# Kernel tuning notes

Measured on AMD Instinct MI355X. Metric: run time of the kernel, lower is better.

Reference implementation:

```python
import jax, jax.numpy as jnp
import numpy as np

B, N, M12, H, O, I, DIFF = 8192, 100, 12, 64, 128, 12, 1.0
TWO_PI = 2.0 * np.pi


def _moments_single(xi, K):
    # xi: [N, 2] single sample; K: [12, 2] exponent pairs -> [12]
    xc = xi - xi.mean(axis=0)                 # center per-sample (mean over points)
    p = xc[:, None, :] ** K[None, :, :]       # [N, 12, 2]
    return jnp.sum(p[..., 0] * p[..., 1], axis=0)  # [12]


def setup_inputs() -> dict:
    key = jax.random.key(0)
    ks = jax.random.split(key, 8)
    # 12 integer central-moment exponent pairs (p, q)
    P = jnp.array([1, 2, 0, 2, 1, 3, 0, 2, 3, 1, 4, 0], jnp.float32)
    Q = jnp.array([1, 0, 2, 1, 2, 0, 3, 2, 1, 3, 0, 4], jnp.float32)
    K = jnp.stack([P, Q], axis=-1)            # [12, 2]

    x = jax.random.normal(ks[0], (B, N, 2), jnp.float32)
    t = jax.random.uniform(ks[1], (1,), jnp.float32, 0.1, 1.0)  # positive time
    W_fourier = jax.random.normal(ks[2], (H // 2,), jnp.float32) * 30.0

    def lin(k, fin, fout):
        bound = 1.0 / np.sqrt(fin)
        kw, kb = jax.random.split(k)
        W = jax.random.uniform(kw, (fin, fout), jnp.float32, -bound, bound)
        b = jax.random.uniform(kb, (fout,), jnp.float32, -bound, bound)
        return W, b

    embed_W, embed_b = lin(ks[3], H, H)
    lin1_W, lin1_b = lin(ks[4], I, H)
    lin2a_W, lin2a_b = lin(ks[5], H, O)
    lin2b_W, lin2b_b = lin(ks[6], O, I)
    lin2c_W, lin2c_b = lin(ks[7], I, I)
    return {
        'x': x, 't': t, 'K': K, 'W_fourier': W_fourier,
        'embed_W': embed_W, 'embed_b': embed_b,
        'lin1_W': lin1_W, 'lin1_b': lin1_b,
        'lin2a_W': lin2a_W, 'lin2a_b': lin2a_b,
        'lin2b_W': lin2b_W, 'lin2b_b': lin2b_b,
        'lin2c_W': lin2c_W, 'lin2c_b': lin2c_b,
    }


def reference(x, t, K, W_fourier, embed_W, embed_b, lin1_W, lin1_b,
              lin2a_W, lin2a_b, lin2b_W, lin2b_b, lin2c_W, lin2c_b):
    # Invariance encoding ('Moment' mode): [B, 12]
    m = jax.vmap(_moments_single, in_axes=(0, None))(x, K)
    h = jax.nn.gelu(m @ lin1_W + lin1_b, approximate=False)   # [B, H] (dropout = eval identity)
    # Gaussian Fourier time embedding: [1, H]
    xp = t[:, None] * W_fourier[None, :] * TWO_PI
    emb = jnp.concatenate([jnp.sin(xp), jnp.cos(xp)], axis=-1) @ embed_W + embed_b
    h = jax.nn.gelu((h + emb) @ lin2a_W + lin2a_b, approximate=False)
    h = jax.nn.gelu(h @ lin2b_W + lin2b_b, approximate=False)
    h = (h @ lin2c_W + lin2c_b) / jnp.sqrt(DIFF * t)          # [B, 12]
    # Per-sample jacobian of the moment map: [B, 12, N, 2]
    # (equals the block diagonal of torch.autograd.functional.jacobian over the batch)
    jac = jax.vmap(jax.jacrev(_moments_single), in_axes=(0, None))(x, K)
    # Replaces the (i, j) double loop of tiny matmuls with one batched contraction
    return jnp.einsum('bk,bknj->bnj', h, jac)                 # [B, N, 2]
```

## Files before the change

kernel.cpp:

```cpp
#include <hip/hip_runtime.h>
#include <hip/hip_bf16.h>


static __device__ __forceinline__ float gelu_f(float x) {
    float y = 0.7071067811865475f * x;
    float s = fabsf(y);
    float t = __builtin_amdgcn_rcpf(fmaf(0.3275911f, s, 1.0f));
    float p = t * fmaf(t, fmaf(t, fmaf(t, fmaf(t, 1.061405429f,
                    -1.453152027f), 1.421413741f), -0.284496736f), 0.254829592f);
    float e = __expf(-y * y);
    float ea = fmaf(-p, e, 1.0f);
    float erfv = copysignf(ea, y);
    return 0.5f * x * (1.0f + erfv);
}

#define DPP_ADD(v, ctrl) \
    v += __int_as_float(__builtin_amdgcn_update_dpp(0, __float_as_int(v), ctrl, 0xf, 0xf, true))

static __device__ __forceinline__ float wave_sum(float v) {
    DPP_ADD(v, 0x111);
    DPP_ADD(v, 0x112);
    DPP_ADD(v, 0x114);
    DPP_ADD(v, 0x118);
    DPP_ADD(v, 0x142);
    DPP_ADD(v, 0x143);
    return __int_as_float(__builtin_amdgcn_readlane(__float_as_int(v), 63));
}

#define TWO_PI_F 6.283185307179586f

__global__ __launch_bounds__(256) void scorenet_fused(
    const float* __restrict__ x,
    const float* __restrict__ t_in,
    const float* __restrict__ Wf,
    const float* __restrict__ embW,
    const float* __restrict__ embB,
    const float* __restrict__ W1,
    const float* __restrict__ b1,
    const float* __restrict__ W2a,
    const float* __restrict__ b2a,
    const float* __restrict__ W2b,
    const float* __restrict__ b2b,
    const float* __restrict__ W2c,
    const float* __restrict__ b2c,
    float* __restrict__ out,
    int B)
{
    __shared__ float s_f[64];
    __shared__ float s_emb[64];

    const int tid = threadIdx.x;
    const float tval = t_in[0];

    if (tid < 32) {
        float xp = tval * Wf[tid] * TWO_PI_F;
        s_f[tid]      = sinf(xp);
        s_f[tid + 32] = cosf(xp);
    }
    __syncthreads();
    if (tid < 64) {
        float acc = embB[tid];
        const float4* f4 = reinterpret_cast<const float4*>(s_f);
        #pragma unroll
        for (int c = 0; c < 16; ++c) {
            float4 a4 = f4[c];
            int j = 4 * c;
            acc = fmaf(a4.x, embW[(j+0)*64 + tid],
                  fmaf(a4.y, embW[(j+1)*64 + tid],
                  fmaf(a4.z, embW[(j+2)*64 + tid],
                  fmaf(a4.w, embW[(j+3)*64 + tid], acc))));
        }
        s_emb[tid] = acc;
    }
    __syncthreads();

    const int lane = tid & 63;
    const int b = blockIdx.x * 4 + (tid >> 6);
    if (b >= B) return;

    const float2* px = reinterpret_cast<const float2*>(x) + (size_t)b * 100;
    const bool has2 = lane < 36;

    float2 p0 = px[lane];
    float2 p1 = px[has2 ? lane + 64 : lane];
    float xa = p0.x, ya = p0.y;
    float xb = has2 ? p1.x : 0.0f;
    float yb = has2 ? p1.y : 0.0f;

    const float mux = wave_sum(xa + xb) * 0.01f;
    const float muy = wave_sum(ya + yb) * 0.01f;

    float ua = xa - mux, va = ya - muy;
    float ub = has2 ? (xb - mux) : 0.0f;
    float vb = has2 ? (yb - muy) : 0.0f;

    float ms[12];
    {
        float u2 = ua * ua, v2 = va * va;
        ms[0] = ua * va;   ms[1] = u2;        ms[2] = v2;
        ms[3] = u2 * va;   ms[4] = ua * v2;
        ms[5] = u2 * ua;   ms[6] = v2 * va;
        ms[7] = u2 * v2;   ms[8] = ms[5] * va; ms[9] = ua * ms[6];
        ms[10] = u2 * u2;  ms[11] = v2 * v2;
        float w2 = ub * ub, z2 = vb * vb;
        ms[0] += ub * vb;  ms[1] += w2;       ms[2] += z2;
        ms[3] += w2 * vb;  ms[4] += ub * z2;
        ms[5] += w2 * ub;  ms[6] += z2 * vb;
        ms[7] += w2 * z2;  ms[8] += w2 * ub * vb; ms[9] += ub * z2 * vb;
        ms[10] += w2 * w2; ms[11] += z2 * z2;
    }
    float m[12];
    #pragma unroll
    for (int k = 0; k < 12; ++k) m[k] = wave_sum(ms[k]);

    float a1 = b1[lane];
    #pragma unroll
    for (int k = 0; k < 12; ++k) a1 = fmaf(m[k], W1[k * 64 + lane], a1);
    float aval = gelu_f(a1) + s_emb[lane];

    float acc0 = b2a[lane];
    float acc1 = b2a[lane + 64];
    #pragma unroll
    for (int j = 0; j < 64; ++j) {
        float aj = __int_as_float(__builtin_amdgcn_readlane(__float_as_int(aval), j));
        acc0 = fmaf(aj, W2a[j * 128 + lane], acc0);
        acc1 = fmaf(aj, W2a[j * 128 + 64 + lane], acc1);
    }
    float h2lo = gelu_f(acc0), h2hi = gelu_f(acc1);

    float h3[12];
    #pragma unroll
    for (int k = 0; k < 12; ++k) {
        float p3 = fmaf(h2lo, W2b[lane * 12 + k], h2hi * W2b[(lane + 64) * 12 + k]);
        h3[k] = gelu_f(wave_sum(p3) + b2b[k]);
    }

    const float rst = rsqrtf(tval);
    float h[12];
    #pragma unroll
    for (int k = 0; k < 12; ++k) {
        float acc = b2c[k];
        #pragma unroll
        for (int j = 0; j < 12; ++j) acc = fmaf(h3[j], W2c[j * 12 + k], acc);
        h[k] = acc * rst;
    }

    const float inv_n = 0.01f;
    float c0 = (2.0f*h[3]*m[0] + h[4]*m[2] + 3.0f*h[5]*m[1] + 2.0f*h[7]*m[4]
              + 3.0f*h[8]*m[3] + h[9]*m[6] + 4.0f*h[10]*m[5]) * inv_n;
    float c1 = (h[3]*m[1] + 2.0f*h[4]*m[0] + 3.0f*h[6]*m[2] + 2.0f*h[7]*m[3]
              + h[8]*m[5] + 3.0f*h[9]*m[4] + 4.0f*h[11]*m[6]) * inv_n;

    const float A1 = 2.0f*h[1], A2 = h[0],      A3 = 3.0f*h[5], A4 = 2.0f*h[3], A5 = h[4];
    const float A6 = 4.0f*h[10],A7 = 3.0f*h[8], A8 = 2.0f*h[7], A9 = h[9];
    const float B1 = h[0],      B2 = 2.0f*h[2], B3 = h[3],      B4 = 2.0f*h[4], B5 = 3.0f*h[6];
    const float B6 = h[8],      B7 = 2.0f*h[7], B8 = 3.0f*h[9], B9 = 4.0f*h[11];

    float2* pout = reinterpret_cast<float2*>(out) + (size_t)b * 100;
    {
        float u = ua, v = va;
        float u2 = u*u, v2 = v*v;
        float o0 = A1*u + A2*v + A3*u2 + A4*u*v + A5*v2 + A6*u2*u + A7*u2*v + A8*u*v2 + A9*v2*v - c0;
        float o1 = B1*u + B2*v + B3*u2 + B4*u*v + B5*v2 + B6*u2*u + B7*u2*v + B8*u*v2 + B9*v2*v - c1;
        float2 r; r.x = o0; r.y = o1;
        pout[lane] = r;
    }
    if (has2) {
        float u = ub, v = vb;
        float u2 = u*u, v2 = v*v;
        float o0 = A1*u + A2*v + A3*u2 + A4*u*v + A5*v2 + A6*u2*u + A7*u2*v + A8*u*v2 + A9*v2*v - c0;
        float o1 = B1*u + B2*v + B3*u2 + B4*u*v + B5*v2 + B6*u2*u + B7*u2*v + B8*u*v2 + B9*v2*v - c1;
        float2 r; r.x = o0; r.y = o1;
        pout[lane + 64] = r;
    }
}

extern "C" void kernel_launch(void* const* d_in, const int* in_sizes, int n_in,
                              void* d_out, int out_size, void* d_ws, size_t ws_size,
                              hipStream_t stream) {
    const float* x    = (const float*)d_in[0];
    const float* t    = (const float*)d_in[1];
    const float* Wf   = (const float*)d_in[3];
    const float* embW = (const float*)d_in[4];
    const float* embB = (const float*)d_in[5];
    const float* W1   = (const float*)d_in[6];
    const float* b1   = (const float*)d_in[7];
    const float* W2a  = (const float*)d_in[8];
    const float* b2a  = (const float*)d_in[9];
    const float* W2b  = (const float*)d_in[10];
    const float* b2b  = (const float*)d_in[11];
    const float* W2c  = (const float*)d_in[12];
    const float* b2c  = (const float*)d_in[13];

    const int B = in_sizes[0] / 200;
    const int blocks = (B + 3) / 4;

    scorenet_fused<<<blocks, 256, 0, stream>>>(
        x, t, Wf, embW, embB, W1, b1, W2a, b2a, W2b, b2b, W2c, b2c,
        (float*)d_out, B);
}
```

Baseline: 101.2 us.

## Share W2a loads across block's four samples via LDS split-K, hoist x loads

Restructures the 64x128 layer so each wave handles a quarter of the K dimension for all four samples in the block. Activations are staged in shared memory and partial sums are reduced through LDS, which cuts per-sample W2a global loads by four. The x loads are moved ahead of the Fourier embedding setup so they overlap it. W2b is read with float4 loads, and the final 12x12 layer is computed one output per lane and then broadcast with readlane. The cost is extra barriers and about 8KB of LDS, and out-of-range waves now stay alive to reach the barriers.

```diff
diff --git a/kernel.cpp b/kernel.cpp
--- a/kernel.cpp
+++ b/kernel.cpp
@@ -1,5 +1,4 @@
 #include <hip/hip_runtime.h>
-#include <hip/hip_bf16.h>
 
 
 static __device__ __forceinline__ float gelu_f(float x) {
@@ -48,9 +47,22 @@
 {
     __shared__ float s_f[64];
     __shared__ float s_emb[64];
+    __shared__ float s_a[64][4];
+    __shared__ float s_part[4][2][4][64];
 
     const int tid = threadIdx.x;
+    const int lane = tid & 63;
+    const int w = tid >> 6;
     const float tval = t_in[0];
+
+    const int b = blockIdx.x * 4 + w;
+    const bool valid = b < B;
+    const int bc = valid ? b : B - 1;
+
+    const float2* px = reinterpret_cast<const float2*>(x) + (size_t)bc * 100;
+    const bool has2 = lane < 36;
+    float2 p0 = px[lane];
+    float2 p1 = px[has2 ? lane + 64 : lane];
 
     if (tid < 32) {
         float xp = tval * Wf[tid] * TWO_PI_F;
@@ -74,15 +86,6 @@
     }
     __syncthreads();
 
-    const int lane = tid & 63;
-    const int b = blockIdx.x * 4 + (tid >> 6);
-    if (b >= B) return;
-
-    const float2* px = reinterpret_cast<const float2*>(x) + (size_t)b * 100;
-    const bool has2 = lane < 36;
-
-    float2 p0 = px[lane];
-    float2 p1 = px[has2 ? lane + 64 : lane];
     float xa = p0.x, ya = p0.y;
     float xb = has2 ? p1.x : 0.0f;
     float yb = has2 ? p1.y : 0.0f;
@@ -118,32 +121,70 @@
     for (int k = 0; k < 12; ++k) a1 = fmaf(m[k], W1[k * 64 + lane], a1);
     float aval = gelu_f(a1) + s_emb[lane];
 
-    float acc0 = b2a[lane];
-    float acc1 = b2a[lane + 64];
-    #pragma unroll
-    for (int j = 0; j < 64; ++j) {
-        float aj = __int_as_float(__builtin_amdgcn_readlane(__float_as_int(aval), j));
-        acc0 = fmaf(aj, W2a[j * 128 + lane], acc0);
-        acc1 = fmaf(aj, W2a[j * 128 + 64 + lane], acc1);
-    }
+    s_a[lane][w] = aval;
+    __syncthreads();
+
+    float4 plo = {0.f, 0.f, 0.f, 0.f};
+    float4 phi = {0.f, 0.f, 0.f, 0.f};
+    {
+        const float4* a4p = reinterpret_cast<const float4*>(&s_a[0][0]);
+        const float2* w2a2 = reinterpret_cast<const float2*>(W2a);
+        #pragma unroll
+        for (int jj = 0; jj < 16; ++jj) {
+            const int j = (w << 4) + jj;
+            float4 a4 = a4p[j];
+            float2 ww = w2a2[j * 64 + lane];
+            plo.x = fmaf(a4.x, ww.x, plo.x);
+            plo.y = fmaf(a4.y, ww.x, plo.y);
+            plo.z = fmaf(a4.z, ww.x, plo.z);
+            plo.w = fmaf(a4.w, ww.x, plo.w);
+            phi.x = fmaf(a4.x, ww.y, phi.x);
+            phi.y = fmaf(a4.y, ww.y, phi.y);
+            phi.z = fmaf(a4.z, ww.y, phi.z);
+            phi.w = fmaf(a4.w, ww.y, phi.w);
+        }
+    }
+    s_part[0][0][w][lane] = plo.x;
+    s_part[1][0][w][lane] = plo.y;
+    s_part[2][0][w][lane] = plo.z;
+    s_part[3][0][w][lane] = plo.w;
+    s_part[0][1][w][lane] = phi.x;
+    s_part[1][1][w][lane] = phi.y;
+    s_part[2][1][w][lane] = phi.z;
+    s_part[3][1][w][lane] = phi.w;
+    __syncthreads();
+
+    const float2 bb2a = reinterpret_cast<const float2*>(b2a)[lane];
+    float acc0 = bb2a.x + ((s_part[w][0][0][lane] + s_part[w][0][1][lane])
+                         + (s_part[w][0][2][lane] + s_part[w][0][3][lane]));
+    float acc1 = bb2a.y + ((s_part[w][1][0][lane] + s_part[w][1][1][lane])
+                         + (s_part[w][1][2][lane] + s_part[w][1][3][lane]));
     float h2lo = gelu_f(acc0), h2hi = gelu_f(acc1);
 
+    const float4* w2b4 = reinterpret_cast<const float4*>(W2b);
+    float4 l0 = w2b4[lane * 6 + 0], l1 = w2b4[lane * 6 + 1], l2 = w2b4[lane * 6 + 2];
+    float4 u0 = w2b4[lane * 6 + 3], u1 = w2b4[lane * 6 + 4], u2 = w2b4[lane * 6 + 5];
+    const float wl[12] = {l0.x,l0.y,l0.z,l0.w, l1.x,l1.y,l1.z,l1.w, l2.x,l2.y,l2.z,l2.w};
+    const float wu[12] = {u0.x,u0.y,u0.z,u0.w, u1.x,u1.y,u1.z,u1.w, u2.x,u2.y,u2.z,u2.w};
     float h3[12];
     #pragma unroll
     for (int k = 0; k < 12; ++k) {
-        float p3 = fmaf(h2lo, W2b[lane * 12 + k], h2hi * W2b[(lane + 64) * 12 + k]);
+        float p3 = fmaf(h2lo, wl[k], h2hi * wu[k]);
         h3[k] = gelu_f(wave_sum(p3) + b2b[k]);
     }
 
     const float rst = rsqrtf(tval);
+    float hk = 0.0f;
+    if (lane < 12) {
+        hk = b2c[lane];
+        #pragma unroll
+        for (int j = 0; j < 12; ++j) hk = fmaf(h3[j], W2c[j * 12 + lane], hk);
+        hk *= rst;
+    }
     float h[12];
     #pragma unroll
-    for (int k = 0; k < 12; ++k) {
-        float acc = b2c[k];
-        #pragma unroll
-        for (int j = 0; j < 12; ++j) acc = fmaf(h3[j], W2c[j * 12 + k], acc);
-        h[k] = acc * rst;
-    }
+    for (int k = 0; k < 12; ++k)
+        h[k] = __int_as_float(__builtin_amdgcn_readlane(__float_as_int(hk), k));
 
     const float inv_n = 0.01f;
     float c0 = (2.0f*h[3]*m[0] + h[4]*m[2] + 3.0f*h[5]*m[1] + 2.0f*h[7]*m[4]
@@ -156,22 +197,22 @@
     const float B1 = h[0],      B2 = 2.0f*h[2], B3 = h[3],      B4 = 2.0f*h[4], B5 = 3.0f*h[6];
     const float B6 = h[8],      B7 = 2.0f*h[7], B8 = 3.0f*h[9], B9 = 4.0f*h[11];
 
-    float2* pout = reinterpret_cast<float2*>(out) + (size_t)b * 100;
-    {
+    float2* pout = reinterpret_cast<float2*>(out) + (size_t)bc * 100;
+    if (valid) {
         float u = ua, v = va;
         float u2 = u*u, v2 = v*v;
         float o0 = A1*u + A2*v + A3*u2 + A4*u*v + A5*v2 + A6*u2*u + A7*u2*v + A8*u*v2 + A9*v2*v - c0;
         float o1 = B1*u + B2*v + B3*u2 + B4*u*v + B5*v2 + B6*u2*u + B7*u2*v + B8*u*v2 + B9*v2*v - c1;
         float2 r; r.x = o0; r.y = o1;
         pout[lane] = r;
-    }
-    if (has2) {
-        float u = ub, v = vb;
-        float u2 = u*u, v2 = v*v;
-        float o0 = A1*u + A2*v + A3*u2 + A4*u*v + A5*v2 + A6*u2*u + A7*u2*v + A8*u*v2 + A9*v2*v - c0;
-        float o1 = B1*u + B2*v + B3*u2 + B4*u*v + B5*v2 + B6*u2*u + B7*u2*v + B8*u*v2 + B9*v2*v - c1;
-        float2 r; r.x = o0; r.y = o1;
-        pout[lane + 64] = r;
+        if (has2) {
+            float uu = ub, vv = vb;
+            float uu2 = uu*uu, vv2 = vv*vv;
+            float q0 = A1*uu + A2*vv + A3*uu2 + A4*uu*vv + A5*vv2 + A6*uu2*uu + A7*uu2*vv + A8*uu*vv2 + A9*vv2*vv - c0;
+            float q1 = B1*uu + B2*vv + B3*uu2 + B4*uu*vv + B5*vv2 + B6*uu2*uu + B7*uu2*vv + B8*uu*vv2 + B9*vv2*vv - c1;
+            float2 r2; r2.x = q0; r2.y = q1;
+            pout[lane + 64] = r2;
+        }
     }
 }
 
```

New measurement: 96.53 us. -4.6%, faster.
